# Optimization experiments

Measured on AMD Instinct MI355X. Metric: run time of the kernel, lower is better.

Reference implementation:

```python
import jax, jax.numpy as jnp
import numpy as np

N = 50000   # nodes
E = 600000  # edges
D = 128     # in_feats == n_hidden


def setup_inputs() -> dict:
    key = jax.random.key(0)
    ks = jax.random.split(key, 10)
    s = 0.1
    return {
        "x": jax.random.normal(ks[0], (N, D), jnp.float32),
        "W1": jax.random.normal(ks[1], (D, D), jnp.float32) * s,
        "b1": jnp.zeros((D,), jnp.float32),
        "W2": jax.random.normal(ks[2], (D, D), jnp.float32) * s,
        "b2": jnp.zeros((D,), jnp.float32),
        "Wp": jax.random.normal(ks[3], (D, D), jnp.float32) * s,
        "bp": jnp.zeros((D,), jnp.float32),
        "edge_src": jax.random.randint(ks[4], (E,), 0, N),
        "edge_dst": jax.random.randint(ks[5], (E,), 0, N),
        "perm": jax.random.randint(ks[6], (N,), 0, N),
    }


def _graph_conv(h, W, b, src, dst, norm):
    # DGL GraphConv (norm='both'): D^-1/2 A D^-1/2 H W + b
    m = h[src] * norm[src, None]                      # [E, D] gather
    agg = jax.ops.segment_sum(m, dst, num_segments=N)  # [N, D] scatter-add
    return (agg * norm[:, None]) @ W + b


def _encode(x, W1, b1, W2, b2, src, dst, norm):
    h = jax.nn.relu(_graph_conv(x, W1, b1, src, dst, norm))
    return _graph_conv(h, W2, b2, src, dst, norm)


def reference(x, W1, b1, W2, b2, Wp, bp, edge_src, edge_dst, perm):
    # symmetric normalization from in-degree (clamped to avoid div by 0)
    deg = jax.ops.segment_sum(jnp.ones((E,), x.dtype), edge_dst, num_segments=N)
    norm = jax.lax.rsqrt(jnp.maximum(deg, 1.0))

    h1 = _encode(x, W1, b1, W2, b2, edge_src, edge_dst, norm)        # clean
    h2 = _encode(x[perm], W1, b1, W2, b2, edge_src, edge_dst, norm)  # corrupt

    sc1 = (h1 @ Wp + bp).sum(axis=1)  # [N]
    sc2 = (h2 @ Wp + bp).sum(axis=1)  # [N]

    logits = jnp.concatenate([sc1, sc2])                   # [2N]
    lbl = jnp.concatenate([jnp.ones((N,), x.dtype), jnp.zeros((N,), x.dtype)])
    # BCEWithLogitsLoss (mean): softplus(z) - z*y  (numerically stable)
    loss = jnp.mean(jax.nn.softplus(logits) - logits * lbl)
    return loss
```

## Files before the change

### kernel.cpp

```cpp
#include <hip/hip_runtime.h>
#include <math.h>

#define D 128

typedef float f32x2 __attribute__((ext_vector_type(2)));
typedef float f32x4 __attribute__((ext_vector_type(4)));
typedef short short8 __attribute__((ext_vector_type(8)));

__device__ __forceinline__ float softplusf(float z){
    return log1pf(expf(-fabsf(z))) + fmaxf(z, 0.f);
}
__device__ __forceinline__ unsigned short f2bf(float f){
    unsigned u = __float_as_uint(f);
    u += 0x7fffu + ((u >> 16) & 1u);
    return (unsigned short)(u >> 16);
}

__global__ void __launch_bounds__(256) k_clear(int* __restrict__ deg, int N,
                                               int* __restrict__ accblk){
    int i = blockIdx.x*blockDim.x + threadIdx.x;
    int i4 = i*4;
    if (i4 + 3 < N) *(int4*)&deg[i4] = make_int4(0,0,0,0);
    else { for (int q=0;q<4;++q) if (i4+q < N) deg[i4+q] = 0; }
    if (i < 64) accblk[i] = 0;
}

__global__ void __launch_bounds__(256) k_prep(
    const float* __restrict__ W1, unsigned short* __restrict__ wf,
    const float* __restrict__ W2, const float* __restrict__ b2,
    const float* __restrict__ Wp, const float* __restrict__ bp,
    float* __restrict__ v, float* __restrict__ cconst)
{
    __shared__ float wps[D];
    const int b = blockIdx.x;
    const int tid = threadIdx.x;
    if (b < 8){
        int kc = tid >> 6, l = tid & 63;
        int c  = b*16 + (l & 15);
        int kb = kc*32 + (l >> 4)*8;
        union { unsigned short us[8]; short8 s; } uu;
        #pragma unroll
        for (int j = 0; j < 8; ++j) uu.us[j] = f2bf(W1[(size_t)(kb+j)*D + c]);
        *(short8*)&wf[((size_t)(b*4 + kc)*64 + l)*8] = uu.s;
    } else {
        int lane = tid & 63, wid = tid >> 6;
        for (int r = wid; r < D; r += 4){
            float a = Wp[(size_t)r*D + lane] + Wp[(size_t)r*D + 64 + lane];
            for (int off=32; off>0; off>>=1) a += __shfl_down(a, off);
            if (lane == 0) wps[r] = a;
        }
        __syncthreads();
        float wl0 = wps[lane], wl1 = wps[64 + lane];
        for (int r = wid; r < D; r += 4){
            float a = W2[(size_t)r*D + lane]*wl0 + W2[(size_t)r*D + 64 + lane]*wl1;
            for (int off=32; off>0; off>>=1) a += __shfl_down(a, off);
            if (lane == 0) v[r] = a;
        }
        if (wid == 0){
            float a = b2[lane]*wl0 + b2[64+lane]*wl1 + bp[lane] + bp[64+lane];
            for (int off=32; off>0; off>>=1) a += __shfl_down(a, off);
            if (lane == 0) cconst[0] = a;
        }
    }
}

__global__ void __launch_bounds__(256) k_fused1(
    const float* __restrict__ x, const unsigned short* __restrict__ wf,
    unsigned* __restrict__ xw8, int N,
    const int* __restrict__ edst, int* __restrict__ deg, int E, int nGemm)
{
    const int b = blockIdx.x;
    const int tid = threadIdx.x;
    if (b < nGemm){
        const int l = tid & 63, w = tid >> 6;
        const int r  = b*64 + w*16 + (l & 15);
        const int kb = (l >> 4) * 8;
        short8 a[4];
        #pragma unroll
        for (int kc = 0; kc < 4; ++kc){
            float4 f0 = make_float4(0.f,0.f,0.f,0.f), f1 = f0;
            if (r < N){
                const float* px = &x[(size_t)r*D + kc*32 + kb];
                f0 = *(const float4*)px;
                f1 = *(const float4*)(px + 4);
            }
            unsigned u0,u1,u2,u3;
            asm("v_cvt_pk_bf16_f32 %0, %1, %2" : "=v"(u0) : "v"(f0.x), "v"(f0.y));
            asm("v_cvt_pk_bf16_f32 %0, %1, %2" : "=v"(u1) : "v"(f0.z), "v"(f0.w));
            asm("v_cvt_pk_bf16_f32 %0, %1, %2" : "=v"(u2) : "v"(f1.x), "v"(f1.y));
            asm("v_cvt_pk_bf16_f32 %0, %1, %2" : "=v"(u3) : "v"(f1.z), "v"(f1.w));
            union { unsigned u[4]; short8 s; } uu = {{u0, u1, u2, u3}};
            a[kc] = uu.s;
        }
        const short8* __restrict__ wfr = (const short8*)wf;
        #pragma unroll
        for (int nt = 0; nt < 8; ++nt){
            f32x4 acc = {0.f, 0.f, 0.f, 0.f};
            #pragma unroll
            for (int kc = 0; kc < 4; ++kc)
                acc = __builtin_amdgcn_mfma_f32_16x16x32_bf16(
                          wfr[(nt*4 + kc)*64 + l], a[kc], acc, 0, 0, 0);
            int pk = __builtin_amdgcn_cvt_pk_fp8_f32(acc[0], acc[1], 0, false);
            pk     = __builtin_amdgcn_cvt_pk_fp8_f32(acc[2], acc[3], pk, true);
            if (r < N) xw8[(size_t)r*32 + nt*4 + (l >> 4)] = (unsigned)pk;
        }
    } else {
        int e = (b - nGemm)*256 + tid;
        if (e < E) atomicAdd(&deg[edst[e]], 1);
    }
}

__global__ void k_scanA(const int* __restrict__ deg, int* __restrict__ offs,
                        int* __restrict__ bsum, int N){
    __shared__ int wsums[16];
    __shared__ int gtot;
    int tid = threadIdx.x, lane = tid & 63, wid = tid >> 6;
    int g = blockIdx.x*1024 + tid;
    int val = (g < N) ? deg[g] : 0;
    int inc = val;
    #pragma unroll
    for (int off=1; off<64; off<<=1){
        int t = __shfl_up(inc, off);
        if (lane >= off) inc += t;
    }
    if (lane == 63) wsums[wid] = inc;
    __syncthreads();
    if (wid == 0 && lane < 16){
        int t = wsums[lane];
        int i2 = t;
        #pragma unroll
        for (int off=1; off<16; off<<=1){
            int u = __shfl_up(i2, off);
            if (lane >= off) i2 += u;
        }
        wsums[lane] = i2 - t;
        if (lane == 15) gtot = i2;
    }
    __syncthreads();
    if (g < N) offs[g] = wsums[wid] + inc - val;
    if (tid == 0) bsum[blockIdx.x] = gtot;
}

__global__ void k_scanC(int* __restrict__ offs, const int* __restrict__ bsum,
                        int* __restrict__ cursor, const int* __restrict__ deg,
                        float* __restrict__ norm, int2* __restrict__ ep,
                        const int* __restrict__ perm, int N){
    __shared__ int sbase;
    int tid = threadIdx.x;
    if (tid < 64){
        int val = (tid < (int)blockIdx.x) ? bsum[tid] : 0;
        for (int off=32; off>0; off>>=1) val += __shfl_down(val, off);
        if (tid == 0) sbase = val;
    }
    __syncthreads();
    int g = blockIdx.x*1024 + tid;
    if (g < N){
        int o = offs[g] + sbase;
        offs[g] = o;
        cursor[g] = o;
        float nm = rsqrtf(fmaxf((float)deg[g], 1.f));
        norm[g] = nm;
        ep[g] = make_int2(perm[g], __float_as_int(nm));
    }
}

__global__ void k_fill(const int* __restrict__ src, const int* __restrict__ dst,
                       int* __restrict__ cursor, const int2* __restrict__ ep,
                       int2* __restrict__ epe, int E){
    int e = blockIdx.x*blockDim.x + threadIdx.x;
    if (e < E){
        int s  = src[e];
        int dd = dst[e];
        int p  = atomicAdd(&cursor[dd], 1);
        int2 eo = ep[s];
        epe[p] = make_int2(s | (eo.x << 16), eo.y);
    }
}

#define FMA8(u, nk) { \
    f32x2 f01 = __builtin_amdgcn_cvt_pk_f32_fp8((int)(u), false); \
    f32x2 f23 = __builtin_amdgcn_cvt_pk_f32_fp8((int)(u), true);  \
    ac.x = fmaf(f01.x, (nk), ac.x); ac.y = fmaf(f01.y, (nk), ac.y); \
    ac.z = fmaf(f23.x, (nk), ac.z); ac.w = fmaf(f23.y, (nk), ac.w); }

__global__ void __launch_bounds__(256) k_agg(const unsigned* __restrict__ xw8,
                     const int2* __restrict__ epe, const int* __restrict__ offs,
                     const int* __restrict__ deg, const float* __restrict__ norm,
                     const float* __restrict__ b1,
                     const float* __restrict__ v, float2* __restrict__ t2, int N){
    int w = threadIdx.x >> 6;
    int lane = threadIdx.x & 63;
    int i = blockIdx.x*4 + w;
    if (i >= N) return;
    int half = lane >> 5;
    int sh = half << 4;
    int c = lane & 31;
    const unsigned* __restrict__ xr = xw8;
    float4 ac = make_float4(0.f,0.f,0.f,0.f);
    int start = offs[i], cnt = deg[i];

    for (int base = 0; base < cnt; base += 64){
        int m = min(cnt - base, 64);
        int ssp = 0; float ns = 0.f;
        if (lane < m){
            int2 t = epe[start + base + lane];
            ssp = t.x;
            ns = __int_as_float(t.y);
        }
        int k = 0;
        for (; k + 4 <= m; k += 4){
            int p0=__shfl(ssp,k  ); float n0=__shfl(ns,k  );
            int p1=__shfl(ssp,k+1); float n1=__shfl(ns,k+1);
            int p2=__shfl(ssp,k+2); float n2=__shfl(ns,k+2);
            int p3=__shfl(ssp,k+3); float n3=__shfl(ns,k+3);
            unsigned r0 = ((unsigned)p0 >> sh) & 0xffffu;
            unsigned r1 = ((unsigned)p1 >> sh) & 0xffffu;
            unsigned r2 = ((unsigned)p2 >> sh) & 0xffffu;
            unsigned r3 = ((unsigned)p3 >> sh) & 0xffffu;
            unsigned d0 = xr[(size_t)r0*32 + c];
            unsigned d1 = xr[(size_t)r1*32 + c];
            unsigned d2 = xr[(size_t)r2*32 + c];
            unsigned d3 = xr[(size_t)r3*32 + c];
            FMA8(d0, n0); FMA8(d1, n1); FMA8(d2, n2); FMA8(d3, n3);
        }
        for (; k < m; ++k){
            int pk_=__shfl(ssp,k); float nk=__shfl(ns,k);
            unsigned r = ((unsigned)pk_ >> sh) & 0xffffu;
            unsigned dv = xr[(size_t)r*32 + c];
            FMA8(dv, nk);
        }
    }
    float ni = norm[i];
    float4 bb = ((const float4*)b1)[c];
    float4 vv = ((const float4*)v)[c];
    float p = fmaxf(fmaf(ac.x, ni, bb.x), 0.f)*vv.x
            + fmaxf(fmaf(ac.y, ni, bb.y), 0.f)*vv.y
            + fmaxf(fmaf(ac.z, ni, bb.z), 0.f)*vv.z
            + fmaxf(fmaf(ac.w, ni, bb.w), 0.f)*vv.w;
    for (int off=16; off>0; off>>=1) p += __shfl_xor(p, off);
    float pd = __shfl(p, 32);
    if (lane == 0) t2[i] = make_float2(ni*p, ni*pd);
}

__global__ void k_loss(const float2* __restrict__ t2, const int2* __restrict__ epe,
                       const int* __restrict__ offs, const int* __restrict__ deg,
                       const float* __restrict__ norm, const float* __restrict__ cconst,
                       float* __restrict__ acc, unsigned* __restrict__ done,
                       float* __restrict__ out, int N, int nblocks){
    int i = blockIdx.x*blockDim.x + threadIdx.x;
    float li = 0.f;
    if (i < N){
        int start = offs[i], cnt = deg[i];
        float sc = 0.f, sd = 0.f;
        for (int k=0;k<cnt;k++){
            int s = epe[start+k].x & 0xffff;
            float2 t = t2[s];
            sc += t.x; sd += t.y;
        }
        float ni = norm[i], C = cconst[0];
        li = softplusf(-fmaf(ni, sc, C)) + softplusf(fmaf(ni, sd, C));
    }
    for (int off=32; off>0; off>>=1) li += __shfl_down(li, off);
    __shared__ float wsum[4];
    int lane = threadIdx.x & 63, wid = threadIdx.x >> 6;
    if (lane == 0) wsum[wid] = li;
    __syncthreads();
    if (threadIdx.x == 0){
        float s = wsum[0] + wsum[1] + wsum[2] + wsum[3];
        atomicAdd(acc, s);
        __threadfence();
        unsigned t = atomicAdd(done, 1u);
        if (t == (unsigned)(nblocks - 1)){
            float tot = atomicAdd(acc, 0.0f);
            out[0] = tot / (float)(2*N);
        }
    }
}

extern "C" void kernel_launch(void* const* d_in, const int* in_sizes, int n_in,
                              void* d_out, int out_size, void* d_ws, size_t ws_size,
                              hipStream_t stream){
    const float* x    = (const float*)d_in[0];
    const float* W1   = (const float*)d_in[1];
    const float* b1   = (const float*)d_in[2];
    const float* W2   = (const float*)d_in[3];
    const float* b2   = (const float*)d_in[4];
    const float* Wp   = (const float*)d_in[5];
    const float* bp   = (const float*)d_in[6];
    const int*   esrc = (const int*)d_in[7];
    const int*   edst = (const int*)d_in[8];
    const int*   perm = (const int*)d_in[9];
    const int N = in_sizes[0] / D;
    const int E = in_sizes[7];

    char* ws = (char*)d_ws;
    size_t off = 0;
    auto alloc = [&](size_t bytes)->void*{
        void* p = ws + off;
        off += (bytes + 255) & ~(size_t)255;
        return p;
    };
    unsigned* xw8 = (unsigned*)alloc((size_t)N*32*sizeof(unsigned));
    unsigned short* wf = (unsigned short*)alloc((size_t)D*D*sizeof(unsigned short));
    int*   deg    = (int*)  alloc((size_t)N*sizeof(int));
    float* acc    = (float*)alloc(256);
    unsigned* done = (unsigned*)(acc + 1);
    float* norm   = (float*)alloc((size_t)N*sizeof(float));
    int*   offs   = (int*)  alloc((size_t)N*sizeof(int));
    int*   cursor = (int*)  alloc((size_t)N*sizeof(int));
    int2*  ep     = (int2*) alloc((size_t)N*sizeof(int2));
    int2*  epe    = (int2*) alloc((size_t)E*sizeof(int2));
    float2* t2    = (float2*)alloc((size_t)N*sizeof(float2));
    int*   bsum   = (int*)  alloc(4096);
    float* v      = (float*)alloc(D*sizeof(float));
    float* cconst = (float*)alloc(256);

    int nGemm = (N + 63) / 64;
    int nDeg  = (E + 255) / 256;
    int nb    = (N + 1023) / 1024;
    int nLoss = (N + 255) / 256;
    int nClear = (N/4 + 255) / 256 + 1;

    k_clear <<<nClear, 256, 0, stream>>>(deg, N, (int*)acc);
    k_prep  <<<9, 256, 0, stream>>>(W1, wf, W2, b2, Wp, bp, v, cconst);
    k_fused1<<<nGemm + nDeg, 256, 0, stream>>>(x, wf, xw8, N, edst, deg, E, nGemm);
    k_scanA <<<nb, 1024, 0, stream>>>(deg, offs, bsum, N);
    k_scanC <<<nb, 1024, 0, stream>>>(offs, bsum, cursor, deg, norm, ep, perm, N);
    k_fill  <<<(E+255)/256, 256, 0, stream>>>(esrc, edst, cursor, ep, epe, E);
    k_agg   <<<(N+3)/4, 256, 0, stream>>>(xw8, epe, offs, deg, norm, b1, v, t2, N);
    k_loss  <<<nLoss, 256, 0, stream>>>(t2, epe, offs, deg, norm, cconst, acc, done,
                                        (float*)d_out, N, nLoss);
}
```

Before: 156.7 us.

## Fuse all pipeline stages into one cooperative persistent kernel with grid syncs

```diff
diff --git a/kernel.cpp b/kernel.cpp
--- a/kernel.cpp
+++ b/kernel.cpp
@@ -1,7 +1,11 @@
 #include <hip/hip_runtime.h>
+#include <hip/hip_cooperative_groups.h>
 #include <math.h>
 
+namespace cg = cooperative_groups;
+
 #define D 128
+#define BT 256
 
 typedef float f32x2 __attribute__((ext_vector_type(2)));
 typedef float f32x4 __attribute__((ext_vector_type(4)));
@@ -14,6 +18,249 @@
     unsigned u = __float_as_uint(f);
     u += 0x7fffu + ((u >> 16) & 1u);
     return (unsigned short)(u >> 16);
+}
+
+#define FMA8(u, nk) { \
+    f32x2 f01 = __builtin_amdgcn_cvt_pk_f32_fp8((int)(u), false); \
+    f32x2 f23 = __builtin_amdgcn_cvt_pk_f32_fp8((int)(u), true);  \
+    ac.x = fmaf(f01.x, (nk), ac.x); ac.y = fmaf(f01.y, (nk), ac.y); \
+    ac.z = fmaf(f23.x, (nk), ac.z); ac.w = fmaf(f23.y, (nk), ac.w); }
+
+__global__ void __launch_bounds__(256) k_mega(
+    const float* __restrict__ x, const float* __restrict__ W1,
+    const float* __restrict__ b1, const float* __restrict__ W2,
+    const float* __restrict__ b2, const float* __restrict__ Wp,
+    const float* __restrict__ bp, const int* __restrict__ esrc,
+    const int* __restrict__ edst, const int* __restrict__ perm,
+    unsigned* __restrict__ xw8, unsigned short* __restrict__ wf,
+    int* __restrict__ deg, float* __restrict__ acc,
+    float* __restrict__ norm, int* __restrict__ offs, int* __restrict__ cursor,
+    int2* __restrict__ ep, int2* __restrict__ epe, float2* __restrict__ t2,
+    int* __restrict__ bsum, float* __restrict__ v, float* __restrict__ cconst,
+    float* __restrict__ out, int N, int E, int nGemm, int nDeg, int nb)
+{
+    cg::grid_group grid = cg::this_grid();
+    const int b = blockIdx.x, tid = threadIdx.x, G = gridDim.x;
+    const int lane = tid & 63, wid = tid >> 6;
+    __shared__ float s_wps[D];
+    __shared__ int   s_wsums[4];
+    __shared__ float s_fsum[4];
+
+    for (int i4 = (b*BT + tid)*4; i4 < N; i4 += G*BT*4){
+        if (i4 + 3 < N) *(int4*)&deg[i4] = make_int4(0,0,0,0);
+        else { for (int q=0;q<4;++q) if (i4+q < N) deg[i4+q] = 0; }
+    }
+    if (b == 9 && tid < 64) ((int*)acc)[tid] = 0;
+    if (b < 8){
+        int kc = wid & 3;
+        int c  = b*16 + (lane & 15);
+        int kb = kc*32 + (lane >> 4)*8;
+        union { unsigned short us[8]; short8 s; } uu;
+        #pragma unroll
+        for (int j = 0; j < 8; ++j) uu.us[j] = f2bf(W1[(size_t)(kb+j)*D + c]);
+        *(short8*)&wf[((size_t)(b*4 + kc)*64 + lane)*8] = uu.s;
+    } else if (b == 8){
+        for (int r = wid; r < D; r += 4){
+            float a = Wp[(size_t)r*D + lane] + Wp[(size_t)r*D + 64 + lane];
+            for (int off=32; off>0; off>>=1) a += __shfl_down(a, off);
+            if (lane == 0) s_wps[r] = a;
+        }
+        __syncthreads();
+        float wl0 = s_wps[lane], wl1 = s_wps[64 + lane];
+        for (int r = wid; r < D; r += 4){
+            float a = W2[(size_t)r*D + lane]*wl0 + W2[(size_t)r*D + 64 + lane]*wl1;
+            for (int off=32; off>0; off>>=1) a += __shfl_down(a, off);
+            if (lane == 0) v[r] = a;
+        }
+        if (wid == 0){
+            float a = b2[lane]*wl0 + b2[64+lane]*wl1 + bp[lane] + bp[64+lane];
+            for (int off=32; off>0; off>>=1) a += __shfl_down(a, off);
+            if (lane == 0) cconst[0] = a;
+        }
+    }
+    grid.sync();
+
+    for (int vb = b; vb < nGemm + nDeg; vb += G){
+        if (vb < nGemm){
+            const int r  = vb*64 + wid*16 + (lane & 15);
+            const int kb = (lane >> 4) * 8;
+            short8 a[4];
+            #pragma unroll
+            for (int kc = 0; kc < 4; ++kc){
+                float4 f0 = make_float4(0.f,0.f,0.f,0.f), f1 = f0;
+                if (r < N){
+                    const float* px = &x[(size_t)r*D + kc*32 + kb];
+                    f0 = *(const float4*)px;
+                    f1 = *(const float4*)(px + 4);
+                }
+                unsigned u0,u1,u2,u3;
+                asm("v_cvt_pk_bf16_f32 %0, %1, %2" : "=v"(u0) : "v"(f0.x), "v"(f0.y));
+                asm("v_cvt_pk_bf16_f32 %0, %1, %2" : "=v"(u1) : "v"(f0.z), "v"(f0.w));
+                asm("v_cvt_pk_bf16_f32 %0, %1, %2" : "=v"(u2) : "v"(f1.x), "v"(f1.y));
+                asm("v_cvt_pk_bf16_f32 %0, %1, %2" : "=v"(u3) : "v"(f1.z), "v"(f1.w));
+                union { unsigned u[4]; short8 s; } uu = {{u0, u1, u2, u3}};
+                a[kc] = uu.s;
+            }
+            const short8* __restrict__ wfr = (const short8*)wf;
+            #pragma unroll
+            for (int nt = 0; nt < 8; ++nt){
+                f32x4 ar = {0.f, 0.f, 0.f, 0.f};
+                #pragma unroll
+                for (int kc = 0; kc < 4; ++kc)
+                    ar = __builtin_amdgcn_mfma_f32_16x16x32_bf16(
+                              wfr[(nt*4 + kc)*64 + lane], a[kc], ar, 0, 0, 0);
+                int pk = __builtin_amdgcn_cvt_pk_fp8_f32(ar[0], ar[1], 0, false);
+                pk     = __builtin_amdgcn_cvt_pk_fp8_f32(ar[2], ar[3], pk, true);
+                if (r < N) xw8[(size_t)r*32 + nt*4 + (lane >> 4)] = (unsigned)pk;
+            }
+        } else {
+            int e = (vb - nGemm)*BT + tid;
+            if (e < E) atomicAdd(&deg[edst[e]], 1);
+        }
+    }
+    grid.sync();
+
+    for (int vb = b; vb < nb; vb += G){
+        int g0 = vb*1024 + tid*4;
+        int4 dv = make_int4(0,0,0,0);
+        if (g0 + 3 < N) dv = *(const int4*)&deg[g0];
+        else {
+            dv.x = (g0   < N) ? deg[g0]   : 0;
+            dv.y = (g0+1 < N) ? deg[g0+1] : 0;
+            dv.z = (g0+2 < N) ? deg[g0+2] : 0;
+            dv.w = (g0+3 < N) ? deg[g0+3] : 0;
+        }
+        int s0 = dv.x, s1 = s0 + dv.y, s2 = s1 + dv.z, s3 = s2 + dv.w;
+        int inc = s3;
+        #pragma unroll
+        for (int off=1; off<64; off<<=1){
+            int t = __shfl_up(inc, off);
+            if (lane >= off) inc += t;
+        }
+        if (lane == 63) s_wsums[wid] = inc;
+        __syncthreads();
+        int wbase = 0;
+        #pragma unroll
+        for (int q = 0; q < 4; ++q) if (q < wid) wbase += s_wsums[q];
+        int texc = wbase + inc - s3;
+        if (g0   < N) offs[g0]   = texc;
+        if (g0+1 < N) offs[g0+1] = texc + s0;
+        if (g0+2 < N) offs[g0+2] = texc + s1;
+        if (g0+3 < N) offs[g0+3] = texc + s2;
+        if (tid == 255) bsum[vb] = wbase + inc;
+        __syncthreads();
+    }
+    grid.sync();
+
+    for (int vb = b; vb < nb; vb += G){
+        int val = (lane < vb) ? bsum[lane] : 0;
+        #pragma unroll
+        for (int off=32; off>0; off>>=1) val += __shfl_down(val, off);
+        int base = __shfl(val, 0);
+        #pragma unroll
+        for (int q = 0; q < 4; ++q){
+            int g = vb*1024 + q*256 + tid;
+            if (g < N){
+                int o = offs[g] + base;
+                offs[g] = o;
+                cursor[g] = o;
+                float nm = rsqrtf(fmaxf((float)deg[g], 1.f));
+                norm[g] = nm;
+                ep[g] = make_int2(perm[g], __float_as_int(nm));
+            }
+        }
+    }
+    grid.sync();
+
+    for (int e = b*BT + tid; e < E; e += G*BT){
+        int s  = esrc[e];
+        int dd = edst[e];
+        int p  = atomicAdd(&cursor[dd], 1);
+        int2 eo = ep[s];
+        epe[p] = make_int2(s | (eo.x << 16), eo.y);
+    }
+    grid.sync();
+
+    {
+        int half = lane >> 5;
+        int sh = half << 4;
+        int c = lane & 31;
+        const unsigned* __restrict__ xr = xw8;
+        for (int vb = b; vb*4 < N; vb += G){
+            int i = vb*4 + wid;
+            if (i < N){
+                float4 ac = make_float4(0.f,0.f,0.f,0.f);
+                int start = offs[i], cnt = deg[i];
+                for (int base = 0; base < cnt; base += 64){
+                    int m = min(cnt - base, 64);
+                    int ssp = 0; float ns = 0.f;
+                    if (lane < m){
+                        int2 t = epe[start + base + lane];
+                        ssp = t.x;
+                        ns = __int_as_float(t.y);
+                    }
+                    int k = 0;
+                    for (; k + 4 <= m; k += 4){
+                        int p0=__shfl(ssp,k  ); float n0=__shfl(ns,k  );
+                        int p1=__shfl(ssp,k+1); float n1=__shfl(ns,k+1);
+                        int p2=__shfl(ssp,k+2); float n2=__shfl(ns,k+2);
+                        int p3=__shfl(ssp,k+3); float n3=__shfl(ns,k+3);
+                        unsigned r0 = ((unsigned)p0 >> sh) & 0xffffu;
+                        unsigned r1 = ((unsigned)p1 >> sh) & 0xffffu;
+                        unsigned r2 = ((unsigned)p2 >> sh) & 0xffffu;
+                        unsigned r3 = ((unsigned)p3 >> sh) & 0xffffu;
+                        unsigned d0 = xr[(size_t)r0*32 + c];
+                        unsigned d1 = xr[(size_t)r1*32 + c];
+                        unsigned d2 = xr[(size_t)r2*32 + c];
+                        unsigned d3 = xr[(size_t)r3*32 + c];
+                        FMA8(d0, n0); FMA8(d1, n1); FMA8(d2, n2); FMA8(d3, n3);
+                    }
+                    for (; k < m; ++k){
+                        int pk_=__shfl(ssp,k); float nk=__shfl(ns,k);
+                        unsigned r = ((unsigned)pk_ >> sh) & 0xffffu;
+                        unsigned dvv = xr[(size_t)r*32 + c];
+                        FMA8(dvv, nk);
+                    }
+                }
+                float ni = norm[i];
+                float4 bb = ((const float4*)b1)[c];
+                float4 vv = ((const float4*)v)[c];
+                float p = fmaxf(fmaf(ac.x, ni, bb.x), 0.f)*vv.x
+                        + fmaxf(fmaf(ac.y, ni, bb.y), 0.f)*vv.y
+                        + fmaxf(fmaf(ac.z, ni, bb.z), 0.f)*vv.z
+                        + fmaxf(fmaf(ac.w, ni, bb.w), 0.f)*vv.w;
+                for (int off=16; off>0; off>>=1) p += __shfl_xor(p, off);
+                float pd = __shfl(p, 32);
+                if (lane == 0) t2[i] = make_float2(ni*p, ni*pd);
+            }
+        }
+    }
+    grid.sync();
+
+    {
+        float li = 0.f;
+        float C = cconst[0];
+        for (int i = b*BT + tid; i < N; i += G*BT){
+            int start = offs[i], cnt = deg[i];
+            float sc = 0.f, sd = 0.f;
+            for (int k=0;k<cnt;k++){
+                int s = epe[start+k].x & 0xffff;
+                float2 t = t2[s];
+                sc += t.x; sd += t.y;
+            }
+            float ni = norm[i];
+            li += softplusf(-fmaf(ni, sc, C)) + softplusf(fmaf(ni, sd, C));
+        }
+        for (int off=32; off>0; off>>=1) li += __shfl_down(li, off);
+        if (lane == 0) s_fsum[wid] = li;
+        __syncthreads();
+        if (tid == 0){
+            float s = s_fsum[0] + s_fsum[1] + s_fsum[2] + s_fsum[3];
+            if (s != 0.f) atomicAdd(acc, s);
+        }
+    }
+    grid.sync();
+    if (b == 0 && tid == 0) out[0] = acc[0] / (float)(2*N);
 }
 
 __global__ void __launch_bounds__(256) k_clear(int* __restrict__ deg, int N,
@@ -176,12 +423,6 @@
         epe[p] = make_int2(s | (eo.x << 16), eo.y);
     }
 }
-
-#define FMA8(u, nk) { \
-    f32x2 f01 = __builtin_amdgcn_cvt_pk_f32_fp8((int)(u), false); \
-    f32x2 f23 = __builtin_amdgcn_cvt_pk_f32_fp8((int)(u), true);  \
-    ac.x = fmaf(f01.x, (nk), ac.x); ac.y = fmaf(f01.y, (nk), ac.y); \
-    ac.z = fmaf(f23.x, (nk), ac.z); ac.w = fmaf(f23.y, (nk), ac.w); }
 
 __global__ void __launch_bounds__(256) k_agg(const unsigned* __restrict__ xw8,
                      const int2* __restrict__ epe, const int* __restrict__ offs,
@@ -314,20 +555,52 @@
     int*   bsum   = (int*)  alloc(4096);
     float* v      = (float*)alloc(D*sizeof(float));
     float* cconst = (float*)alloc(256);
+    float* outp   = (float*)d_out;
 
     int nGemm = (N + 63) / 64;
     int nDeg  = (E + 255) / 256;
     int nb    = (N + 1023) / 1024;
-    int nLoss = (N + 255) / 256;
-    int nClear = (N/4 + 255) / 256 + 1;
-
-    k_clear <<<nClear, 256, 0, stream>>>(deg, N, (int*)acc);
-    k_prep  <<<9, 256, 0, stream>>>(W1, wf, W2, b2, Wp, bp, v, cconst);
-    k_fused1<<<nGemm + nDeg, 256, 0, stream>>>(x, wf, xw8, N, edst, deg, E, nGemm);
-    k_scanA <<<nb, 1024, 0, stream>>>(deg, offs, bsum, N);
-    k_scanC <<<nb, 1024, 0, stream>>>(offs, bsum, cursor, deg, norm, ep, perm, N);
-    k_fill  <<<(E+255)/256, 256, 0, stream>>>(esrc, edst, cursor, ep, epe, E);
-    k_agg   <<<(N+3)/4, 256, 0, stream>>>(xw8, epe, offs, deg, norm, b1, v, t2, N);
-    k_loss  <<<nLoss, 256, 0, stream>>>(t2, epe, offs, deg, norm, cconst, acc, done,
-                                        (float*)d_out, N, nLoss);
-}
+
+    int maxB = 0;
+    hipError_t occErr = hipOccupancyMaxActiveBlocksPerMultiprocessor(
+        &maxB, (const void*)k_mega, BT, 0);
+    int G = 0;
+    if (occErr == hipSuccess && maxB > 0){
+        hipDeviceProp_t prop;
+        int dev = 0;
+        if (hipGetDevice(&dev) == hipSuccess &&
+            hipGetDeviceProperties(&prop, dev) == hipSuccess){
+            G = maxB * prop.multiProcessorCount;
+        }
+    }
+    if (G > 2048) G = 2048;
+
+    bool launched = false;
+    if (G >= 64 && nb <= 64){
+        void* args[] = {
+            (void*)&x, (void*)&W1, (void*)&b1, (void*)&W2, (void*)&b2,
+            (void*)&Wp, (void*)&bp, (void*)&esrc, (void*)&edst, (void*)&perm,
+            (void*)&xw8, (void*)&wf, (void*)&deg, (void*)&acc,
+            (void*)&norm, (void*)&offs, (void*)&cursor, (void*)&ep, (void*)&epe,
+            (void*)&t2, (void*)&bsum, (void*)&v, (void*)&cconst,
+            (void*)&outp, (void*)&N, (void*)&E, (void*)&nGemm, (void*)&nDeg, (void*)&nb
+        };
+        hipError_t err = hipLaunchCooperativeKernel((const void*)k_mega,
+                             dim3(G), dim3(BT), args, 0, stream);
+        launched = (err == hipSuccess);
+    }
+
+    if (!launched){
+        int nLoss = (N + 255) / 256;
+        int nClear = (N/4 + 255) / 256 + 1;
+        k_clear <<<nClear, 256, 0, stream>>>(deg, N, (int*)acc);
+        k_prep  <<<9, 256, 0, stream>>>(W1, wf, W2, b2, Wp, bp, v, cconst);
+        k_fused1<<<nGemm + nDeg, 256, 0, stream>>>(x, wf, xw8, N, edst, deg, E, nGemm);
+        k_scanA <<<nb, 1024, 0, stream>>>(deg, offs, bsum, N);
+        k_scanC <<<nb, 1024, 0, stream>>>(offs, bsum, cursor, deg, norm, ep, perm, N);
+        k_fill  <<<(E+255)/256, 256, 0, stream>>>(esrc, edst, cursor, ep, epe, E);
+        k_agg   <<<(N+3)/4, 256, 0, stream>>>(xw8, epe, offs, deg, norm, b1, v, t2, N);
+        k_loss  <<<nLoss, 256, 0, stream>>>(t2, epe, offs, deg, norm, cconst, acc, done,
+                                            outp, N, nLoss);
+    }
+}
```

New measurement: 582.8 us. 3.72x slower.

## Process four consecutive nodes per wavefront in aggregation kernel

Applied to the files above, without the earlier changes.

```diff
diff --git a/kernel.cpp b/kernel.cpp
--- a/kernel.cpp
+++ b/kernel.cpp
@@ -177,69 +177,87 @@
     }
 }
 
-#define FMA8(u, nk) { \
+#define FMA8A(AC, u, nk) { \
     f32x2 f01 = __builtin_amdgcn_cvt_pk_f32_fp8((int)(u), false); \
     f32x2 f23 = __builtin_amdgcn_cvt_pk_f32_fp8((int)(u), true);  \
-    ac.x = fmaf(f01.x, (nk), ac.x); ac.y = fmaf(f01.y, (nk), ac.y); \
-    ac.z = fmaf(f23.x, (nk), ac.z); ac.w = fmaf(f23.y, (nk), ac.w); }
+    AC.x = fmaf(f01.x, (nk), AC.x); AC.y = fmaf(f01.y, (nk), AC.y); \
+    AC.z = fmaf(f23.x, (nk), AC.z); AC.w = fmaf(f23.y, (nk), AC.w); }
+
+#define PROC_RUN(AC) \
+    for (; k + 4 <= lim; k += 4){ \
+        int q0=__shfl(ssp,k  ), q1=__shfl(ssp,k+1); \
+        int q2=__shfl(ssp,k+2), q3=__shfl(ssp,k+3); \
+        float n0=__shfl(ns,k  ), n1=__shfl(ns,k+1); \
+        float n2=__shfl(ns,k+2), n3=__shfl(ns,k+3); \
+        unsigned r0=((unsigned)q0>>sh)&0xffffu, r1=((unsigned)q1>>sh)&0xffffu; \
+        unsigned r2=((unsigned)q2>>sh)&0xffffu, r3=((unsigned)q3>>sh)&0xffffu; \
+        unsigned d0=xr[(size_t)r0*32+c], d1=xr[(size_t)r1*32+c]; \
+        unsigned d2=xr[(size_t)r2*32+c], d3=xr[(size_t)r3*32+c]; \
+        FMA8A(AC,d0,n0); FMA8A(AC,d1,n1); FMA8A(AC,d2,n2); FMA8A(AC,d3,n3); } \
+    for (; k < lim; ++k){ \
+        int qq=__shfl(ssp,k); float nn=__shfl(ns,k); \
+        unsigned rr=((unsigned)qq>>sh)&0xffffu; \
+        unsigned dd=xr[(size_t)rr*32+c]; \
+        FMA8A(AC,dd,nn); }
 
 __global__ void __launch_bounds__(256) k_agg(const unsigned* __restrict__ xw8,
                      const int2* __restrict__ epe, const int* __restrict__ offs,
                      const int* __restrict__ deg, const float* __restrict__ norm,
-                     const float* __restrict__ b1,
-                     const float* __restrict__ v, float2* __restrict__ t2, int N){
-    int w = threadIdx.x >> 6;
-    int lane = threadIdx.x & 63;
-    int i = blockIdx.x*4 + w;
-    if (i >= N) return;
-    int half = lane >> 5;
-    int sh = half << 4;
+                     const float* __restrict__ b1, const float* __restrict__ v,
+                     float2* __restrict__ t2, int N){
+    int wid = threadIdx.x >> 6, lane = threadIdx.x & 63;
+    int i0 = (blockIdx.x*4 + wid)*4;
+    if (i0 >= N) return;
+    int sh = (lane >> 5) << 4;
     int c = lane & 31;
     const unsigned* __restrict__ xr = xw8;
-    float4 ac = make_float4(0.f,0.f,0.f,0.f);
-    int start = offs[i], cnt = deg[i];
-
-    for (int base = 0; base < cnt; base += 64){
-        int m = min(cnt - base, 64);
+
+    int d0 = deg[i0];
+    int d1 = (i0+1 < N) ? deg[i0+1] : 0;
+    int d2 = (i0+2 < N) ? deg[i0+2] : 0;
+    int d3 = (i0+3 < N) ? deg[i0+3] : 0;
+    int cum1 = d0, cum2 = cum1+d1, cum3 = cum2+d2, total = cum3+d3;
+    int st = offs[i0];
+
+    float4 ac0 = make_float4(0.f,0.f,0.f,0.f), ac1 = ac0, ac2 = ac0, ac3 = ac0;
+    int j = 0;
+    for (int base = 0; base < total; base += 64){
+        int m = min(total - base, 64);
         int ssp = 0; float ns = 0.f;
         if (lane < m){
-            int2 t = epe[start + base + lane];
-            ssp = t.x;
-            ns = __int_as_float(t.y);
+            int2 t = epe[st + base + lane];
+            ssp = t.x; ns = __int_as_float(t.y);
         }
         int k = 0;
-        for (; k + 4 <= m; k += 4){
-            int p0=__shfl(ssp,k  ); float n0=__shfl(ns,k  );
-            int p1=__shfl(ssp,k+1); float n1=__shfl(ns,k+1);
-            int p2=__shfl(ssp,k+2); float n2=__shfl(ns,k+2);
-            int p3=__shfl(ssp,k+3); float n3=__shfl(ns,k+3);
-            unsigned r0 = ((unsigned)p0 >> sh) & 0xffffu;
-            unsigned r1 = ((unsigned)p1 >> sh) & 0xffffu;
-            unsigned r2 = ((unsigned)p2 >> sh) & 0xffffu;
-            unsigned r3 = ((unsigned)p3 >> sh) & 0xffffu;
-            unsigned d0 = xr[(size_t)r0*32 + c];
-            unsigned d1 = xr[(size_t)r1*32 + c];
-            unsigned d2 = xr[(size_t)r2*32 + c];
-            unsigned d3 = xr[(size_t)r3*32 + c];
-            FMA8(d0, n0); FMA8(d1, n1); FMA8(d2, n2); FMA8(d3, n3);
-        }
-        for (; k < m; ++k){
-            int pk_=__shfl(ssp,k); float nk=__shfl(ns,k);
-            unsigned r = ((unsigned)pk_ >> sh) & 0xffffu;
-            unsigned dv = xr[(size_t)r*32 + c];
-            FMA8(dv, nk);
-        }
-    }
-    float ni = norm[i];
+        while (k < m){
+            int cumj1 = (j==0) ? cum1 : (j==1) ? cum2 : (j==2) ? cum3 : total;
+            while (base + k >= cumj1 && j < 3){
+                ++j;
+                cumj1 = (j==1) ? cum2 : (j==2) ? cum3 : total;
+            }
+            int lim = cumj1 - base; if (lim > m) lim = m;
+            switch(j){
+                case 0: { PROC_RUN(ac0) } break;
+                case 1: { PROC_RUN(ac1) } break;
+                case 2: { PROC_RUN(ac2) } break;
+                default:{ PROC_RUN(ac3) } break;
+            }
+        }
+    }
     float4 bb = ((const float4*)b1)[c];
     float4 vv = ((const float4*)v)[c];
-    float p = fmaxf(fmaf(ac.x, ni, bb.x), 0.f)*vv.x
-            + fmaxf(fmaf(ac.y, ni, bb.y), 0.f)*vv.y
-            + fmaxf(fmaf(ac.z, ni, bb.z), 0.f)*vv.z
-            + fmaxf(fmaf(ac.w, ni, bb.w), 0.f)*vv.w;
-    for (int off=16; off>0; off>>=1) p += __shfl_xor(p, off);
-    float pd = __shfl(p, 32);
-    if (lane == 0) t2[i] = make_float2(ni*p, ni*pd);
+    #define EPILOG(Q, AC) \
+        if (i0 + Q < N){ \
+            float ni = norm[i0 + Q]; \
+            float p = fmaxf(fmaf(AC.x, ni, bb.x), 0.f)*vv.x \
+                    + fmaxf(fmaf(AC.y, ni, bb.y), 0.f)*vv.y \
+                    + fmaxf(fmaf(AC.z, ni, bb.z), 0.f)*vv.z \
+                    + fmaxf(fmaf(AC.w, ni, bb.w), 0.f)*vv.w; \
+            for (int off=16; off>0; off>>=1) p += __shfl_xor(p, off); \
+            float pd = __shfl(p, 32); \
+            if (lane == 0) t2[i0 + Q] = make_float2(ni*p, ni*pd); }
+    EPILOG(0, ac0) EPILOG(1, ac1) EPILOG(2, ac2) EPILOG(3, ac3)
+    #undef EPILOG
 }
 
 __global__ void k_loss(const float2* __restrict__ t2, const int2* __restrict__ epe,
@@ -320,6 +338,7 @@
     int nb    = (N + 1023) / 1024;
     int nLoss = (N + 255) / 256;
     int nClear = (N/4 + 255) / 256 + 1;
+    int nAgg  = (N + 15) / 16;
 
     k_clear <<<nClear, 256, 0, stream>>>(deg, N, (int*)acc);
     k_prep  <<<9, 256, 0, stream>>>(W1, wf, W2, b2, Wp, bp, v, cconst);
@@ -327,7 +346,7 @@
     k_scanA <<<nb, 1024, 0, stream>>>(deg, offs, bsum, N);
     k_scanC <<<nb, 1024, 0, stream>>>(offs, bsum, cursor, deg, norm, ep, perm, N);
     k_fill  <<<(E+255)/256, 256, 0, stream>>>(esrc, edst, cursor, ep, epe, E);
-    k_agg   <<<(N+3)/4, 256, 0, stream>>>(xw8, epe, offs, deg, norm, b1, v, t2, N);
+    k_agg   <<<nAgg, 256, 0, stream>>>(xw8, epe, offs, deg, norm, b1, v, t2, N);
     k_loss  <<<nLoss, 256, 0, stream>>>(t2, epe, offs, deg, norm, cconst, acc, done,
                                         (float*)d_out, N, nLoss);
 }
```

After: 157.5 us. About the same (+0.5%).
